# Kernel optimization log

Hardware: AMD Instinct MI355X
Metric: run time of the kernel (lower is better)

## Reference

```python
import jax, jax.numpy as jnp
import numpy as np

DIM = 1024
HEADS = 16
HEAD_DIM = DIM // HEADS


def setup_inputs() -> dict:
    key = jax.random.key(0)
    ks = jax.random.split(key, 9)
    x = jax.random.normal(ks[0], (2, 2048, DIM), dtype=jnp.float32)
    s = 1.0 / np.sqrt(DIM)
    Wq = jax.random.normal(ks[1], (DIM, DIM), dtype=jnp.float32) * s
    bq = jax.random.normal(ks[2], (DIM,), dtype=jnp.float32) * s
    Wk = jax.random.normal(ks[3], (DIM, DIM), dtype=jnp.float32) * s
    bk = jax.random.normal(ks[4], (DIM,), dtype=jnp.float32) * s
    Wv = jax.random.normal(ks[5], (DIM, DIM), dtype=jnp.float32) * s
    bv = jax.random.normal(ks[6], (DIM,), dtype=jnp.float32) * s
    Wo = jax.random.normal(ks[7], (DIM, DIM), dtype=jnp.float32) * s
    bo = jax.random.normal(ks[8], (DIM,), dtype=jnp.float32) * s
    return {"x": x, "Wq": Wq, "bq": bq, "Wk": Wk, "bk": bk,
            "Wv": Wv, "bv": bv, "Wo": Wo, "bo": bo}


def reference(x, Wq, bq, Wk, bk, Wv, bv, Wo, bo):
    B, S, _ = x.shape
    # projections (torch Linear: x @ W.T + b; here W stored as [in, out])
    q = x @ Wq + bq
    k = x @ Wk + bk  # context = x (self-attention)
    v = x @ Wv + bv
    # [B, H, S, Dh]
    q = q.reshape(B, S, HEADS, HEAD_DIM).transpose(0, 2, 1, 3)
    k = k.reshape(B, S, HEADS, HEAD_DIM).transpose(0, 2, 1, 3)
    v = v.reshape(B, S, HEADS, HEAD_DIM).transpose(0, 2, 1, 3)
    scores = jnp.einsum('bhqd,bhkd->bhqk', q, k) / np.sqrt(HEAD_DIM).astype(np.float32)
    weights = jax.nn.softmax(scores, axis=-1)
    emb = jnp.einsum('bhqk,bhkd->bhqd', weights, v)
    emb = emb.transpose(0, 2, 1, 3).reshape(B, S, DIM)
    return emb @ Wo + bo
```

## Files before the change

kernel.cpp:

```cpp
#include <hip/hip_runtime.h>
#include <hip/hip_bf16.h>
#include <stdint.h>

typedef __attribute__((ext_vector_type(8))) short short8;
typedef __attribute__((ext_vector_type(4))) float f32x4;
typedef __attribute__((ext_vector_type(4))) unsigned int uint4v;

#define DIMW 1024
#define HEADS 16
#define HEAD_DIM 64
#define SEQ 2048
#define BATCH 2
#define MTOK 4096
#define QKVN 3072
#define QKN 2048
#define QSCALE 0.1803368801111204f

typedef const __attribute__((address_space(1))) unsigned int* gas_u32p;
typedef __attribute__((address_space(3))) unsigned int* las_u32p;

static __device__ __forceinline__ void gl_lds16(const void* g, void* l) {
    __builtin_amdgcn_global_load_lds((gas_u32p)g, (las_u32p)l, 16, 0, 0);
}

static __device__ __forceinline__ unsigned short f2bf(float f) {
    unsigned int u = __float_as_uint(f);
    u += 0x7fffu + ((u >> 16) & 1u);
    return (unsigned short)(u >> 16);
}

__global__ void cast_x_kernel(const float* __restrict__ x, unsigned short* __restrict__ out) {
    int i = (blockIdx.x * 256 + threadIdx.x) * 8;
    float4 a = *(const float4*)(x + i);
    float4 b = *(const float4*)(x + i + 4);
    unsigned short t[8] = { f2bf(a.x), f2bf(a.y), f2bf(a.z), f2bf(a.w),
                            f2bf(b.x), f2bf(b.y), f2bf(b.z), f2bf(b.w) };
    *(uint4v*)(out + i) = *(const uint4v*)t;
}

__global__ void prep_w_kernel(const float* __restrict__ Wq, const float* __restrict__ Wk,
                              const float* __restrict__ Wv, const float* __restrict__ Wo,
                              unsigned short* __restrict__ Wqkv_t, unsigned short* __restrict__ Wo_t) {
    __shared__ float tile[64][68];
    int z = blockIdx.z;
    const float* W = (z == 0) ? Wq : (z == 1) ? Wk : (z == 2) ? Wv : Wo;
    unsigned short* out = (z < 3) ? (Wqkv_t + (size_t)z * DIMW * DIMW) : Wo_t;
    int n0 = blockIdx.x * 64, k0 = blockIdx.y * 64;
    int tid = threadIdx.x;
    for (int it = 0; it < 4; ++it) {
        int c = it * 256 + tid;
        int r = c >> 4, cg = c & 15;
        float4 v = *(const float4*)(W + (size_t)(k0 + r) * DIMW + n0 + cg * 4);
        tile[r][cg * 4 + 0] = v.x; tile[r][cg * 4 + 1] = v.y;
        tile[r][cg * 4 + 2] = v.z; tile[r][cg * 4 + 3] = v.w;
    }
    __syncthreads();
    for (int it = 0; it < 2; ++it) {
        int c = it * 256 + tid;
        int n = c >> 3, kg = c & 7;
        unsigned short tmp[8];
        #pragma unroll
        for (int j = 0; j < 8; ++j) tmp[j] = f2bf(tile[kg * 8 + j][n]);
        *(uint4v*)(out + (size_t)(n0 + n) * DIMW + k0 + kg * 8) = *(const uint4v*)tmp;
    }
}

template<int MI, bool QKV3, typename TO>
__global__ __launch_bounds__(256, 3) void gemm_bt_kernel(
    const unsigned short* __restrict__ A, const unsigned short* __restrict__ Bt,
    const float* __restrict__ b0, const float* __restrict__ b1, const float* __restrict__ b2,
    TO* __restrict__ C, unsigned short* __restrict__ Vt, int M, int N, int K, int ldc)
{
    __shared__ __align__(16) unsigned short As[MI * 32 * 32];
    __shared__ __align__(16) unsigned short Bs[128 * 32];
    int tid = threadIdx.x;
    int wave = tid >> 6, lane = tid & 63;
    int lrow = lane & 15, quad = lane >> 4;
    int lin = blockIdx.x + gridDim.x * blockIdx.y;
    int cpx = (gridDim.x * gridDim.y) >> 3;
    int v = (lin & 7) * cpx + (lin >> 3);
    int bn_i = v % gridDim.x, bm_i = v / gridDim.x;
    int bm = bm_i * (MI * 32), bn = bn_i * 128;
    int wm = (wave >> 1) * (MI * 16), wn = (wave & 1) * 64;
    int sw = (lrow >> 1) & 3;
    f32x4 acc[MI][4];
    #pragma unroll
    for (int i = 0; i < MI; ++i)
        #pragma unroll
        for (int j = 0; j < 4; ++j) acc[i][j] = (f32x4){0.f, 0.f, 0.f, 0.f};
    const unsigned short* Ap = A + (size_t)bm * K;
    const unsigned short* Bp = Bt + (size_t)bn * K;

    auto stage = [&](int k0) {
        #pragma unroll
        for (int it = 0; it < MI / 2; ++it) {
            int c = it * 256 + tid;
            int ch = (c & 3) ^ ((c >> 3) & 3);
            gl_lds16(Ap + (size_t)(c >> 2) * K + k0 + ch * 8, &As[c * 8]);
        }
        #pragma unroll
        for (int it = 0; it < 2; ++it) {
            int c = it * 256 + tid;
            int ch = (c & 3) ^ ((c >> 3) & 3);
            gl_lds16(Bp + (size_t)(c >> 2) * K + k0 + ch * 8, &Bs[c * 8]);
        }
    };

    stage(0);
    for (int k0 = 0; k0 < K; k0 += 32) {
        asm volatile("s_waitcnt vmcnt(0)" ::: "memory");
        __builtin_amdgcn_sched_barrier(0);
        __builtin_amdgcn_s_barrier();
        short8 af[MI], bfr[4];
        #pragma unroll
        for (int mi = 0; mi < MI; ++mi)
            af[mi] = *(const short8*)&As[(wm + mi * 16 + lrow) * 32 + (quad ^ sw) * 8];
        #pragma unroll
        for (int ni = 0; ni < 4; ++ni)
            bfr[ni] = *(const short8*)&Bs[(wn + ni * 16 + lrow) * 32 + (quad ^ sw) * 8];
        asm volatile("s_waitcnt lgkmcnt(0)" ::: "memory");
        __builtin_amdgcn_sched_barrier(0);
        __builtin_amdgcn_s_barrier();
        if (k0 + 32 < K) stage(k0 + 32);
        __builtin_amdgcn_s_setprio(1);
        #pragma unroll
        for (int mi = 0; mi < MI; ++mi)
            #pragma unroll
            for (int ni = 0; ni < 4; ++ni)
                acc[mi][ni] = __builtin_amdgcn_mfma_f32_16x16x32_bf16(af[mi], bfr[ni], acc[mi][ni], 0, 0, 0);
        __builtin_amdgcn_s_setprio(0);
    }
    #pragma unroll
    for (int ni = 0; ni < 4; ++ni) {
        int n = bn + wn + ni * 16 + lrow;
        float bias, scale;
        int sel = 0;
        if (QKV3) {
            sel = n >> 10;
            const float* bp = (sel == 0) ? b0 : (sel == 1) ? b1 : b2;
            bias = bp[n & 1023];
            scale = (sel == 0) ? QSCALE : 1.0f;
        } else { bias = b0[n]; scale = 1.0f; }
        #pragma unroll
        for (int mi = 0; mi < MI; ++mi) {
            int m0 = bm + wm + mi * 16 + quad * 4;
            if (QKV3 && sel == 2) {
                int vcol = n - 2048;
                int bb = m0 >> 11, s0 = m0 & 2047;
                unsigned short t[4];
                #pragma unroll
                for (int i = 0; i < 4; ++i) t[i] = f2bf(acc[mi][ni][i] + bias);
                *(uint2*)(Vt + ((size_t)(bb * 1024 + vcol)) * SEQ + s0) = *(const uint2*)t;
            } else {
                #pragma unroll
                for (int i = 0; i < 4; ++i) {
                    float val = (acc[mi][ni][i] + bias) * scale;
                    if constexpr (sizeof(TO) == 2) C[(size_t)(m0 + i) * ldc + n] = (TO)f2bf(val);
                    else                           C[(size_t)(m0 + i) * ldc + n] = val;
                }
            }
        }
    }
}

__global__ __launch_bounds__(256, 3) void attn_kernel(
    const unsigned short* __restrict__ Qk, const unsigned short* __restrict__ Vt,
    unsigned short* __restrict__ Op, float* __restrict__ L)
{
    __shared__ __align__(16) unsigned short Ks[128 * 64];
    __shared__ __align__(16) unsigned short Vs[64 * 128];
    int tid = threadIdx.x;
    int wave = tid >> 6, lane = tid & 63;
    int lrow = lane & 15, quad = lane >> 4;
    int h = blockIdx.x, qblk = blockIdx.y;
    int b = blockIdx.z >> 1, split = blockIdx.z & 1;
    int q0 = qblk * 128 + wave * 32;
    const unsigned short* Qbase = Qk + (size_t)(b * SEQ) * QKN + h * 64;
    const unsigned short* Kbase = Qk + (size_t)(b * SEQ) * QKN + 1024 + h * 64;
    const unsigned short* Vtb = Vt + (size_t)(b * 1024 + h * 64) * SEQ;

    short8 qf[2][2];
    #pragma unroll
    for (int mi = 0; mi < 2; ++mi)
        #pragma unroll
        for (int kc = 0; kc < 2; ++kc)
            qf[mi][kc] = *(const short8*)(Qbase + (size_t)(q0 + mi * 16 + lrow) * QKN + kc * 32 + quad * 8);

    short8 ones;
    #pragma unroll
    for (int j = 0; j < 8; ++j) ones[j] = (short)0x3F80;

    f32x4 o[2][4];
    f32x4 lacc[2];
    #pragma unroll
    for (int mi = 0; mi < 2; ++mi) {
        lacc[mi] = (f32x4){0.f, 0.f, 0.f, 0.f};
        #pragma unroll
        for (int ont = 0; ont < 4; ++ont) o[mi][ont] = (f32x4){0.f, 0.f, 0.f, 0.f};
    }

    int kchunk = ((lane & 7) ^ (lane >> 3)) * 8;
    int swk = lrow & 7;

    auto stageK = [&](int kv) {
        #pragma unroll
        for (int it = 0; it < 4; ++it) {
            int r0 = wave * 32 + it * 8;
            gl_lds16(Kbase + (size_t)(kv + r0 + (lane >> 3)) * QKN + kchunk,
                     &Ks[r0 * 64 + lane * 8]);
        }
    };

    int vs_s = lane & 15;
    int vh0 = ((vs_s & 12) << 1) | (vs_s & 3);
    uint2 vreg[8];
    auto loadV = [&](int kv) {
        #pragma unroll
        for (int r = 0; r < 4; ++r) {
            int d = wave * 16 + r * 4 + (lane >> 4);
            const unsigned short* p = Vtb + (size_t)d * SEQ + kv;
            vreg[r * 2]     = *(const uint2*)(p + vh0 * 4);
            vreg[r * 2 + 1] = *(const uint2*)(p + (vh0 + 4) * 4);
        }
    };
    auto writeVs = [&]() {
        #pragma unroll
        for (int r = 0; r < 4; ++r) {
            int d = wave * 16 + r * 4 + (lane >> 4);
            int pos = vs_s ^ (d & 15);
            *(uint2*)&Vs[d * 128 + pos * 8]     = vreg[r * 2];
            *(uint2*)&Vs[d * 128 + pos * 8 + 4] = vreg[r * 2 + 1];
        }
    };

    int kv_lo = split * 1024;
    int kv_end = kv_lo + 1024;

    stageK(kv_lo);
    loadV(kv_lo);
    asm volatile("s_waitcnt vmcnt(0)" ::: "memory");
    __builtin_amdgcn_sched_barrier(0);
    writeVs();

    for (int kv0 = kv_lo; kv0 < kv_end; kv0 += 128) {
        bool has_next = (kv0 + 128) < kv_end;

        __builtin_amdgcn_s_barrier();

        if (has_next) loadV(kv0 + 128);

        uint4v pav[2][4];

        {
            f32x4 s[2][4];
            #pragma unroll
            for (int mi = 0; mi < 2; ++mi)
                #pragma unroll
                for (int nt2 = 0; nt2 < 4; ++nt2) s[mi][nt2] = (f32x4){0.f, 0.f, 0.f, 0.f};
            __builtin_amdgcn_s_setprio(1);
            #pragma unroll
            for (int nt2 = 0; nt2 < 4; ++nt2) {
                int r = nt2 * 16 + lrow;
                short8 kf0 = *(const short8*)&Ks[r * 64 + (quad ^ swk) * 8];
                short8 kf1 = *(const short8*)&Ks[r * 64 + ((4 + quad) ^ swk) * 8];
                #pragma unroll
                for (int mi = 0; mi < 2; ++mi) {
                    s[mi][nt2] = __builtin_amdgcn_mfma_f32_16x16x32_bf16(kf0, qf[mi][0], s[mi][nt2], 0, 0, 0);
                    s[mi][nt2] = __builtin_amdgcn_mfma_f32_16x16x32_bf16(kf1, qf[mi][1], s[mi][nt2], 0, 0, 0);
                }
            }
            __builtin_amdgcn_s_setprio(0);
            #pragma unroll
            for (int mi = 0; mi < 2; ++mi)
                #pragma unroll
                for (int nt2 = 0; nt2 < 4; ++nt2) {
                    f32x4 p;
                    #pragma unroll
                    for (int c2 = 0; c2 < 4; ++c2) p[c2] = __builtin_amdgcn_exp2f(s[mi][nt2][c2]);
                    __hip_bfloat162 a01 = __float22bfloat162_rn(float2{p[0], p[1]});
                    __hip_bfloat162 a23 = __float22bfloat162_rn(float2{p[2], p[3]});
                    if (nt2 & 1) {
                        pav[mi][nt2 >> 1].z = *reinterpret_cast<unsigned int*>(&a01);
                        pav[mi][nt2 >> 1].w = *reinterpret_cast<unsigned int*>(&a23);
                    } else {
                        pav[mi][nt2 >> 1].x = *reinterpret_cast<unsigned int*>(&a01);
                        pav[mi][nt2 >> 1].y = *reinterpret_cast<unsigned int*>(&a23);
                    }
                }
        }

        f32x4 s1[2][4];
        {
            #pragma unroll
            for (int mi = 0; mi < 2; ++mi)
                #pragma unroll
                for (int nt2 = 0; nt2 < 4; ++nt2) s1[mi][nt2] = (f32x4){0.f, 0.f, 0.f, 0.f};
            __builtin_amdgcn_s_setprio(1);
            #pragma unroll
            for (int nt2 = 0; nt2 < 4; ++nt2) {
                int r = (4 + nt2) * 16 + lrow;
                short8 kf0 = *(const short8*)&Ks[r * 64 + (quad ^ swk) * 8];
                short8 kf1 = *(const short8*)&Ks[r * 64 + ((4 + quad) ^ swk) * 8];
                #pragma unroll
                for (int mi = 0; mi < 2; ++mi) {
                    s1[mi][nt2] = __builtin_amdgcn_mfma_f32_16x16x32_bf16(kf0, qf[mi][0], s1[mi][nt2], 0, 0, 0);
                    s1[mi][nt2] = __builtin_amdgcn_mfma_f32_16x16x32_bf16(kf1, qf[mi][1], s1[mi][nt2], 0, 0, 0);
                }
            }
            __builtin_amdgcn_s_setprio(0);
        }

        __builtin_amdgcn_s_barrier();

        if (has_next) stageK(kv0 + 128);

        auto expPack1 = [&](int nt2) {
            #pragma unroll
            for (int mi = 0; mi < 2; ++mi) {
                f32x4 p;
                #pragma unroll
                for (int c2 = 0; c2 < 4; ++c2) p[c2] = __builtin_amdgcn_exp2f(s1[mi][nt2][c2]);
                __hip_bfloat162 a01 = __float22bfloat162_rn(float2{p[0], p[1]});
                __hip_bfloat162 a23 = __float22bfloat162_rn(float2{p[2], p[3]});
                if (nt2 & 1) {
                    pav[mi][2 + (nt2 >> 1)].z = *reinterpret_cast<unsigned int*>(&a01);
                    pav[mi][2 + (nt2 >> 1)].w = *reinterpret_cast<unsigned int*>(&a23);
                } else {
                    pav[mi][2 + (nt2 >> 1)].x = *reinterpret_cast<unsigned int*>(&a01);
                    pav[mi][2 + (nt2 >> 1)].y = *reinterpret_cast<unsigned int*>(&a23);
                }
            }
        };
        auto pvStep = [&](int kc) {
            short8 af0 = *(short8*)&pav[0][kc];
            short8 af1 = *(short8*)&pav[1][kc];
            int pos = ((kc * 4 + quad) ^ lrow) * 8;
            __builtin_amdgcn_s_setprio(1);
            #pragma unroll
            for (int ont = 0; ont < 4; ++ont) {
                int rv = ont * 16 + lrow;
                short8 vf = *(const short8*)&Vs[rv * 128 + pos];
                o[0][ont] = __builtin_amdgcn_mfma_f32_16x16x32_bf16(af0, vf, o[0][ont], 0, 0, 0);
                o[1][ont] = __builtin_amdgcn_mfma_f32_16x16x32_bf16(af1, vf, o[1][ont], 0, 0, 0);
            }
            lacc[0] = __builtin_amdgcn_mfma_f32_16x16x32_bf16(af0, ones, lacc[0], 0, 0, 0);
            lacc[1] = __builtin_amdgcn_mfma_f32_16x16x32_bf16(af1, ones, lacc[1], 0, 0, 0);
            __builtin_amdgcn_s_setprio(0);
        };

        expPack1(0);
        expPack1(1);
        pvStep(0);
        expPack1(2);
        expPack1(3);
        pvStep(1);
        pvStep(2);
        pvStep(3);

        __builtin_amdgcn_s_barrier();

        if (has_next) {
            asm volatile("s_waitcnt vmcnt(0)" ::: "memory");
            __builtin_amdgcn_sched_barrier(0);
            writeVs();
        }
    }

    #pragma unroll
    for (int mi = 0; mi < 2; ++mi) {
        #pragma unroll
        for (int ont = 0; ont < 4; ++ont)
            #pragma unroll
            for (int c2 = 0; c2 < 4; ++c2) {
                size_t row = (size_t)((split * 2 + b) * SEQ + q0 + mi * 16 + quad * 4 + c2);
                Op[row * DIMW + h * 64 + ont * 16 + lrow] = f2bf(o[mi][ont][c2]);
            }
        if (lrow == 0)
            #pragma unroll
            for (int c2 = 0; c2 < 4; ++c2)
                L[(((size_t)(split * 2 + b) * 16 + h) * SEQ) + q0 + mi * 16 + quad * 4 + c2] = lacc[mi][c2];
    }
}

__global__ void combine_kernel(const unsigned short* __restrict__ Op,
                               const float* __restrict__ L,
                               unsigned short* __restrict__ Emb)
{
    int e = (blockIdx.x * 256 + threadIdx.x) * 4;
    int row = e >> 10, c = e & 1023, h = c >> 6;
    int b = row >> 11, q = row & 2047;
    float l1 = L[((size_t)(0 + b) * 16 + h) * SEQ + q];
    float l2 = L[((size_t)(2 + b) * 16 + h) * SEQ + q];
    float inv = 1.0f / (l1 + l2);
    uint2 o1 = *(const uint2*)(Op + e);
    uint2 o2 = *(const uint2*)(Op + 4194304 + e);
    unsigned short t[4];
    unsigned int parts1[4] = { o1.x << 16, o1.x & 0xffff0000u, o1.y << 16, o1.y & 0xffff0000u };
    unsigned int parts2[4] = { o2.x << 16, o2.x & 0xffff0000u, o2.y << 16, o2.y & 0xffff0000u };
    #pragma unroll
    for (int j = 0; j < 4; ++j) {
        float f1 = __uint_as_float(parts1[j]);
        float f2 = __uint_as_float(parts2[j]);
        t[j] = f2bf((f1 + f2) * inv);
    }
    *(uint2*)(Emb + e) = *(const uint2*)t;
}

extern "C" void kernel_launch(void* const* d_in, const int* in_sizes, int n_in,
                              void* d_out, int out_size, void* d_ws, size_t ws_size,
                              hipStream_t stream)
{
    const float* x  = (const float*)d_in[0];
    const float* Wq = (const float*)d_in[1];
    const float* bq = (const float*)d_in[2];
    const float* Wk = (const float*)d_in[3];
    const float* bk = (const float*)d_in[4];
    const float* Wv = (const float*)d_in[5];
    const float* bv = (const float*)d_in[6];
    const float* Wo = (const float*)d_in[7];
    const float* bo = (const float*)d_in[8];
    float* out = (float*)d_out;
    char* ws = (char*)d_ws;

    unsigned short* Xbf   = (unsigned short*)(ws);
    unsigned short* Wqkvt = (unsigned short*)(ws + 8388608);
    unsigned short* Wot   = (unsigned short*)(ws + 14680064);
    unsigned short* Qk    = (unsigned short*)(ws + 16777216);
    unsigned short* Vt    = (unsigned short*)(ws + 33554432);
    unsigned short* Emb   = (unsigned short*)(ws + 41943040);
    unsigned short* Op    = (unsigned short*)(ws + 50331648);
    float*          L     = (float*)(ws + 67108864);

    cast_x_kernel<<<2048, 256, 0, stream>>>(x, Xbf);
    prep_w_kernel<<<dim3(16, 16, 4), 256, 0, stream>>>(Wq, Wk, Wv, Wo, Wqkvt, Wot);
    gemm_bt_kernel<4, true, unsigned short><<<dim3(24, 32), 256, 0, stream>>>(
        Xbf, Wqkvt, bq, bk, bv, Qk, Vt, MTOK, QKVN, DIMW, QKN);
    attn_kernel<<<dim3(16, 16, 4), 256, 0, stream>>>(Qk, Vt, Op, L);
    combine_kernel<<<4096, 256, 0, stream>>>(Op, L, Emb);
    gemm_bt_kernel<4, false, float><<<dim3(8, 32), 256, 0, stream>>>(
        Emb, Wot, bo, nullptr, nullptr, out, nullptr, MTOK, DIMW, DIMW, DIMW);
}
```

Before: 196.4 us.

## Fuse split-KV combine into output GEMM A-load and merge x cast into weight prep

Removes the separate combine kernel by having the output projection GEMM read both split partial outputs, normalize them with per-row/head inverse sums precomputed into shared memory, and write bf16 A tiles to LDS through registers. Also folds the x-to-bf16 cast into the weight prep kernel as extra z-slices, saving a launch. This removes an intermediate Emb round-trip and two launches, but the A path now uses register loads instead of direct global-to-LDS loads. It also does extra ALU work inside the GEMM main loop and adds a prologue that loads L.

Result: slower. 208.7 us (+6.3%).

```diff
diff --git a/kernel.cpp b/kernel.cpp
--- a/kernel.cpp
+++ b/kernel.cpp
@@ -29,24 +29,26 @@
     return (unsigned short)(u >> 16);
 }
 
-__global__ void cast_x_kernel(const float* __restrict__ x, unsigned short* __restrict__ out) {
-    int i = (blockIdx.x * 256 + threadIdx.x) * 8;
-    float4 a = *(const float4*)(x + i);
-    float4 b = *(const float4*)(x + i + 4);
-    unsigned short t[8] = { f2bf(a.x), f2bf(a.y), f2bf(a.z), f2bf(a.w),
-                            f2bf(b.x), f2bf(b.y), f2bf(b.z), f2bf(b.w) };
-    *(uint4v*)(out + i) = *(const uint4v*)t;
-}
-
-__global__ void prep_w_kernel(const float* __restrict__ Wq, const float* __restrict__ Wk,
+__global__ void prep_w_kernel(const float* __restrict__ x, unsigned short* __restrict__ Xbf,
+                              const float* __restrict__ Wq, const float* __restrict__ Wk,
                               const float* __restrict__ Wv, const float* __restrict__ Wo,
                               unsigned short* __restrict__ Wqkv_t, unsigned short* __restrict__ Wo_t) {
     __shared__ float tile[64][68];
     int z = blockIdx.z;
+    int tid = threadIdx.x;
+    if (z >= 4) {
+        int bid = (z - 4) * 256 + blockIdx.y * 16 + blockIdx.x;
+        int i = (bid * 256 + tid) * 8;
+        float4 a = *(const float4*)(x + i);
+        float4 b = *(const float4*)(x + i + 4);
+        unsigned short t[8] = { f2bf(a.x), f2bf(a.y), f2bf(a.z), f2bf(a.w),
+                                f2bf(b.x), f2bf(b.y), f2bf(b.z), f2bf(b.w) };
+        *(uint4v*)(Xbf + i) = *(const uint4v*)t;
+        return;
+    }
     const float* W = (z == 0) ? Wq : (z == 1) ? Wk : (z == 2) ? Wv : Wo;
     unsigned short* out = (z < 3) ? (Wqkv_t + (size_t)z * DIMW * DIMW) : Wo_t;
     int n0 = blockIdx.x * 64, k0 = blockIdx.y * 64;
-    int tid = threadIdx.x;
     for (int it = 0; it < 4; ++it) {
         int c = it * 256 + tid;
         int r = c >> 4, cg = c & 15;
@@ -65,14 +67,17 @@
     }
 }
 
-template<int MI, bool QKV3, typename TO>
+template<int MI, bool QKV3, bool COMBINE, typename TO>
 __global__ __launch_bounds__(256, 3) void gemm_bt_kernel(
     const unsigned short* __restrict__ A, const unsigned short* __restrict__ Bt,
     const float* __restrict__ b0, const float* __restrict__ b1, const float* __restrict__ b2,
-    TO* __restrict__ C, unsigned short* __restrict__ Vt, int M, int N, int K, int ldc)
+    TO* __restrict__ C, unsigned short* __restrict__ Vt,
+    const unsigned short* __restrict__ OpA, const float* __restrict__ Lp,
+    int M, int N, int K, int ldc)
 {
     __shared__ __align__(16) unsigned short As[MI * 32 * 32];
     __shared__ __align__(16) unsigned short Bs[128 * 32];
+    __shared__ float invs[COMBINE ? 2048 : 1];
     int tid = threadIdx.x;
     int wave = tid >> 6, lane = tid & 63;
     int lrow = lane & 15, quad = lane >> 4;
@@ -91,24 +96,74 @@
     const unsigned short* Ap = A + (size_t)bm * K;
     const unsigned short* Bp = Bt + (size_t)bn * K;
 
-    auto stage = [&](int k0) {
+    if constexpr (COMBINE) {
+        for (int e = tid; e < 2048; e += 256) {
+            int r = e >> 4, hh = e & 15;
+            int m = bm + r, bb = m >> 11, q = m & 2047;
+            float l1 = Lp[((size_t)(bb * 16 + hh)) * SEQ + q];
+            float l2 = Lp[((size_t)((2 + bb) * 16 + hh)) * SEQ + q];
+            invs[e] = 1.0f / (l1 + l2);
+        }
+        __syncthreads();
+    }
+
+    uint4v aReg[2][2];
+    auto stageAIssue = [&](int k0) {
+        #pragma unroll
+        for (int it = 0; it < 2; ++it) {
+            int c = it * 256 + tid;
+            int r = c >> 2, ch = (c & 3) ^ ((c >> 3) & 3);
+            size_t off = (size_t)(bm + r) * DIMW + k0 + ch * 8;
+            aReg[it][0] = *(const uint4v*)(OpA + off);
+            aReg[it][1] = *(const uint4v*)(OpA + 4194304 + off);
+        }
+    };
+    auto stageAWrite = [&](int k0) {
+        #pragma unroll
+        for (int it = 0; it < 2; ++it) {
+            int c = it * 256 + tid;
+            int r = c >> 2, ch = (c & 3) ^ ((c >> 3) & 3);
+            float inv = invs[r * 16 + ((k0 + ch * 8) >> 6)];
+            unsigned short t[8];
+            #pragma unroll
+            for (int j = 0; j < 4; ++j) {
+                unsigned int u1 = aReg[it][0][j], u2 = aReg[it][1][j];
+                float f1a = __uint_as_float(u1 << 16), f1b = __uint_as_float(u1 & 0xffff0000u);
+                float f2a = __uint_as_float(u2 << 16), f2b = __uint_as_float(u2 & 0xffff0000u);
+                t[j * 2]     = f2bf((f1a + f2a) * inv);
+                t[j * 2 + 1] = f2bf((f1b + f2b) * inv);
+            }
+            *(uint4v*)&As[c * 8] = *(const uint4v*)t;
+        }
+    };
+    auto stageB = [&](int k0) {
+        #pragma unroll
+        for (int it = 0; it < 2; ++it) {
+            int c = it * 256 + tid;
+            int ch = (c & 3) ^ ((c >> 3) & 3);
+            gl_lds16(Bp + (size_t)(c >> 2) * K + k0 + ch * 8, &Bs[c * 8]);
+        }
+    };
+    auto stageA_lds = [&](int k0) {
         #pragma unroll
         for (int it = 0; it < MI / 2; ++it) {
             int c = it * 256 + tid;
             int ch = (c & 3) ^ ((c >> 3) & 3);
             gl_lds16(Ap + (size_t)(c >> 2) * K + k0 + ch * 8, &As[c * 8]);
         }
-        #pragma unroll
-        for (int it = 0; it < 2; ++it) {
-            int c = it * 256 + tid;
-            int ch = (c & 3) ^ ((c >> 3) & 3);
-            gl_lds16(Bp + (size_t)(c >> 2) * K + k0 + ch * 8, &Bs[c * 8]);
-        }
-    };
-
-    stage(0);
+    };
+
+    if constexpr (COMBINE) {
+        stageAIssue(0); stageB(0);
+        stageAWrite(0);
+    } else {
+        stageA_lds(0); stageB(0);
+    }
     for (int k0 = 0; k0 < K; k0 += 32) {
-        asm volatile("s_waitcnt vmcnt(0)" ::: "memory");
+        if constexpr (COMBINE)
+            asm volatile("s_waitcnt vmcnt(0) lgkmcnt(0)" ::: "memory");
+        else
+            asm volatile("s_waitcnt vmcnt(0)" ::: "memory");
         __builtin_amdgcn_sched_barrier(0);
         __builtin_amdgcn_s_barrier();
         short8 af[MI], bfr[4];
@@ -121,7 +176,11 @@
         asm volatile("s_waitcnt lgkmcnt(0)" ::: "memory");
         __builtin_amdgcn_sched_barrier(0);
         __builtin_amdgcn_s_barrier();
-        if (k0 + 32 < K) stage(k0 + 32);
+        bool has_next = (k0 + 32 < K);
+        if (has_next) {
+            if constexpr (COMBINE) { stageAIssue(k0 + 32); stageB(k0 + 32); }
+            else { stageA_lds(k0 + 32); stageB(k0 + 32); }
+        }
         __builtin_amdgcn_s_setprio(1);
         #pragma unroll
         for (int mi = 0; mi < MI; ++mi)
@@ -129,6 +188,7 @@
             for (int ni = 0; ni < 4; ++ni)
                 acc[mi][ni] = __builtin_amdgcn_mfma_f32_16x16x32_bf16(af[mi], bfr[ni], acc[mi][ni], 0, 0, 0);
         __builtin_amdgcn_s_setprio(0);
+        if constexpr (COMBINE) if (has_next) stageAWrite(k0 + 32);
     }
     #pragma unroll
     for (int ni = 0; ni < 4; ++ni) {
@@ -382,30 +442,6 @@
     }
 }
 
-__global__ void combine_kernel(const unsigned short* __restrict__ Op,
-                               const float* __restrict__ L,
-                               unsigned short* __restrict__ Emb)
-{
-    int e = (blockIdx.x * 256 + threadIdx.x) * 4;
-    int row = e >> 10, c = e & 1023, h = c >> 6;
-    int b = row >> 11, q = row & 2047;
-    float l1 = L[((size_t)(0 + b) * 16 + h) * SEQ + q];
-    float l2 = L[((size_t)(2 + b) * 16 + h) * SEQ + q];
-    float inv = 1.0f / (l1 + l2);
-    uint2 o1 = *(const uint2*)(Op + e);
-    uint2 o2 = *(const uint2*)(Op + 4194304 + e);
-    unsigned short t[4];
-    unsigned int parts1[4] = { o1.x << 16, o1.x & 0xffff0000u, o1.y << 16, o1.y & 0xffff0000u };
-    unsigned int parts2[4] = { o2.x << 16, o2.x & 0xffff0000u, o2.y << 16, o2.y & 0xffff0000u };
-    #pragma unroll
-    for (int j = 0; j < 4; ++j) {
-        float f1 = __uint_as_float(parts1[j]);
-        float f2 = __uint_as_float(parts2[j]);
-        t[j] = f2bf((f1 + f2) * inv);
-    }
-    *(uint2*)(Emb + e) = *(const uint2*)t;
-}
-
 extern "C" void kernel_launch(void* const* d_in, const int* in_sizes, int n_in,
                               void* d_out, int out_size, void* d_ws, size_t ws_size,
                               hipStream_t stream)
@@ -427,16 +463,13 @@
     unsigned short* Wot   = (unsigned short*)(ws + 14680064);
     unsigned short* Qk    = (unsigned short*)(ws + 16777216);
     unsigned short* Vt    = (unsigned short*)(ws + 33554432);
-    unsigned short* Emb   = (unsigned short*)(ws + 41943040);
     unsigned short* Op    = (unsigned short*)(ws + 50331648);
     float*          L     = (float*)(ws + 67108864);
 
-    cast_x_kernel<<<2048, 256, 0, stream>>>(x, Xbf);
-    prep_w_kernel<<<dim3(16, 16, 4), 256, 0, stream>>>(Wq, Wk, Wv, Wo, Wqkvt, Wot);
-    gemm_bt_kernel<4, true, unsigned short><<<dim3(24, 32), 256, 0, stream>>>(
-        Xbf, Wqkvt, bq, bk, bv, Qk, Vt, MTOK, QKVN, DIMW, QKN);
+    prep_w_kernel<<<dim3(16, 16, 12), 256, 0, stream>>>(x, Xbf, Wq, Wk, Wv, Wo, Wqkvt, Wot);
+    gemm_bt_kernel<4, true, false, unsigned short><<<dim3(24, 32), 256, 0, stream>>>(
+        Xbf, Wqkvt, bq, bk, bv, Qk, Vt, nullptr, nullptr, MTOK, QKVN, DIMW, QKN);
     attn_kernel<<<dim3(16, 16, 4), 256, 0, stream>>>(Qk, Vt, Op, L);
-    combine_kernel<<<4096, 256, 0, stream>>>(Op, L, Emb);
-    gemm_bt_kernel<4, false, float><<<dim3(8, 32), 256, 0, stream>>>(
-        Emb, Wot, bo, nullptr, nullptr, out, nullptr, MTOK, DIMW, DIMW, DIMW);
-}
+    gemm_bt_kernel<4, false, true, float><<<dim3(8, 32), 256, 0, stream>>>(
+        nullptr, Wot, bo, nullptr, nullptr, out, nullptr, Op, L, MTOK, DIMW, DIMW, DIMW);
+}
```
